# Performance work log

Hardware: AMD Instinct MI355X
Metric: run time of the kernel (lower is better)

## Reference

```python
import jax, jax.numpy as jnp
import numpy as np

B, S, D = 2, 2048, 1024
H, HD = 16, 64
MLP = 4096
EPS = 1e-5


def layer_norm(x, g, b):
    mu = jnp.mean(x, axis=-1, keepdims=True)
    var = jnp.mean(jnp.square(x - mu), axis=-1, keepdims=True)
    return (x - mu) * jax.lax.rsqrt(var + EPS) * g + b


def setup_inputs() -> dict:
    key = jax.random.key(0)
    ks = jax.random.split(key, 12)
    s = 0.02
    return {
        "x": jax.random.normal(ks[0], (B, S, D), jnp.float32),
        "ln1_g": jnp.ones((D,), jnp.float32),
        "ln1_b": jnp.zeros((D,), jnp.float32),
        "Wq": jax.random.normal(ks[1], (D, H * HD), jnp.float32) * s,
        "Wk": jax.random.normal(ks[2], (D, H * HD), jnp.float32) * s,
        "Wv": jax.random.normal(ks[3], (D, H * HD), jnp.float32) * s,
        "Wo": jax.random.normal(ks[4], (H * HD, D), jnp.float32) * s,
        "ln2_g": jnp.ones((D,), jnp.float32),
        "ln2_b": jnp.zeros((D,), jnp.float32),
        "fc1_w": jax.random.normal(ks[5], (D, MLP), jnp.float32) * s,
        "fc1_b": jnp.zeros((MLP,), jnp.float32),
        "fc2_w": jax.random.normal(ks[6], (MLP, D), jnp.float32) * s,
        "fc2_b": jnp.zeros((D,), jnp.float32),
    }


def reference(x, ln1_g, ln1_b, Wq, Wk, Wv, Wo, ln2_g, ln2_b, fc1_w, fc1_b, fc2_w, fc2_b):
    b, s, d = x.shape
    scale = 1.0 / np.sqrt(HD)
    h = layer_norm(x, ln1_g, ln1_b)
    # project and split heads: [b, H, s, HD]
    q = (h @ Wq).reshape(b, s, H, HD).transpose(0, 2, 1, 3)
    k = (h @ Wk).reshape(b, s, H, HD).transpose(0, 2, 1, 3)
    v = (h @ Wv).reshape(b, s, H, HD).transpose(0, 2, 1, 3)
    scores = jnp.einsum('bhqd,bhkd->bhqk', q, k) * scale
    causal = jnp.where(jnp.tril(jnp.ones((s, s), bool)), 0.0, -jnp.inf).astype(x.dtype)
    scores = scores + causal[None, None]
    attn_weights = jax.nn.softmax(scores, axis=-1)
    attn_out = jnp.einsum('bhqk,bhkd->bhqd', attn_weights, v)
    attn_out = attn_out.transpose(0, 2, 1, 3).reshape(b, s, H * HD) @ Wo
    x = x + attn_out
    h2 = layer_norm(x, ln2_g, ln2_b)
    mlp = jax.nn.gelu(h2 @ fc1_w + fc1_b, approximate=True) @ fc2_w + fc2_b
    x = x + mlp
    return (x, attn_weights)
```

## Files before the change

kernel.cpp:

```cpp
#include <hip/hip_runtime.h>
#include <cmath>

typedef __bf16 bf16;
typedef __bf16 bf16x8 __attribute__((ext_vector_type(8)));
typedef float f32x4 __attribute__((ext_vector_type(4)));

#define B_ 2
#define S_ 2048
#define D_ 1024
#define H_ 16
#define HD_ 64
#define MLP_ 4096
#define XOUT_ ((size_t)B_ * S_ * D_)

__device__ __forceinline__ void gll16(const void* g, void* l) {
  __builtin_amdgcn_global_load_lds((const __attribute__((address_space(1))) void*)g,
                                   (__attribute__((address_space(3))) void*)l, 16, 0, 0);
}

__device__ __forceinline__ f32x4 mfma16(bf16x8 a, bf16x8 b, f32x4 c) {
  return __builtin_amdgcn_mfma_f32_16x16x32_bf16(a, b, c, 0, 0, 0);
}

__device__ __forceinline__ float bfu2f(unsigned short u) {
  return __uint_as_float(((unsigned int)u) << 16);
}
__device__ __forceinline__ unsigned short f2bu(float v) {
  union { bf16 b; unsigned short u; } c; c.b = (bf16)v; return c.u;
}
__device__ __forceinline__ float ld_sc(const void* p, size_t i, int f32) {
  return f32 ? ((const float*)p)[i] : bfu2f(((const unsigned short*)p)[i]);
}

__global__ __launch_bounds__(64) void detect_k(const unsigned short* __restrict__ x,
                                               int* __restrict__ flag) {
  int tid = threadIdx.x;
  int cnt = 0;
  for (int i = tid; i < 512; i += 64) {
    int e = (x[i] >> 7) & 0xFF;
    if (e >= 0xBF) cnt++;
  }
  #pragma unroll
  for (int d = 1; d < 64; d <<= 1) cnt += __shfl_xor(cnt, d);
  if (tid == 0) flag[0] = (cnt > 8) ? 1 : 0;
}

__global__ __launch_bounds__(256) void transpose_ad(const void* __restrict__ in,
                                                    unsigned short* __restrict__ out,
                                                    int R, int C,
                                                    const int* __restrict__ flagp) {
  __shared__ unsigned short t[64][68];
  const int f32 = flagp[0];
  const int tid = threadIdx.x;
  const int c0 = blockIdx.x * 64, r0 = blockIdx.y * 64;
  for (int i = tid * 4; i < 4096; i += 1024) {
    int rr = i >> 6, cc = i & 63;
    size_t off = (size_t)(r0 + rr) * C + c0 + cc;
    if (f32) {
      float4 f = *(const float4*)((const float*)in + off);
      t[rr][cc + 0] = f2bu(f.x); t[rr][cc + 1] = f2bu(f.y);
      t[rr][cc + 2] = f2bu(f.z); t[rr][cc + 3] = f2bu(f.w);
    } else {
      *(ushort4*)&t[rr][cc] = *(const ushort4*)((const unsigned short*)in + off);
    }
  }
  __syncthreads();
  for (int i = tid * 4; i < 4096; i += 1024) {
    int orr = i & 63, oc = i >> 6;
    ushort4 v;
    v.x = t[orr + 0][oc]; v.y = t[orr + 1][oc];
    v.z = t[orr + 2][oc]; v.w = t[orr + 3][oc];
    *(ushort4*)(out + (size_t)(c0 + oc) * R + r0 + orr) = v;
  }
}

__global__ __launch_bounds__(256) void vtrans_k(const unsigned short* __restrict__ qkv,
                                                unsigned short* __restrict__ vT) {
  __shared__ unsigned short t[64][68];
  const int tid = threadIdx.x;
  const int s0 = blockIdx.x * 64, h = blockIdx.y, b = blockIdx.z;
  for (int i = tid * 4; i < 4096; i += 1024) {
    int si = i >> 6, hd = i & 63;
    *(ushort4*)&t[si][hd] =
        *(const ushort4*)(qkv + (size_t)(b * S_ + s0 + si) * 3072 + 2048 + h * 64 + hd);
  }
  __syncthreads();
  for (int i = tid * 4; i < 4096; i += 1024) {
    int ss = i & 63, hd = i >> 6;
    ushort4 v;
    v.x = t[ss + 0][hd]; v.y = t[ss + 1][hd];
    v.z = t[ss + 2][hd]; v.w = t[ss + 3][hd];
    *(ushort4*)(vT + ((size_t)(b * H_ + h) * 64 + hd) * S_ + s0 + ss) = v;
  }
}

__global__ __launch_bounds__(256) void ln_k(const void* __restrict__ xv,
                                            const void* __restrict__ g,
                                            const void* __restrict__ bvec,
                                            bf16* __restrict__ out,
                                            const int* __restrict__ flagp,
                                            int force_xf32) {
  const int f32 = flagp[0];
  const int xf32 = force_xf32 ? 1 : f32;
  const int row = blockIdx.x, tid = threadIdx.x;
  float v[4];
  if (xf32) {
    float4 f = *(const float4*)((const float*)xv + (size_t)row * 1024 + tid * 4);
    v[0] = f.x; v[1] = f.y; v[2] = f.z; v[3] = f.w;
  } else {
    ushort4 u = *(const ushort4*)((const unsigned short*)xv + (size_t)row * 1024 + tid * 4);
    v[0] = bfu2f(u.x); v[1] = bfu2f(u.y); v[2] = bfu2f(u.z); v[3] = bfu2f(u.w);
  }
  float s = 0.f, q = 0.f;
  #pragma unroll
  for (int i = 0; i < 4; i++) { s += v[i]; q += v[i] * v[i]; }
  #pragma unroll
  for (int d = 1; d < 64; d <<= 1) { s += __shfl_xor(s, d); q += __shfl_xor(q, d); }
  __shared__ float red[8];
  if ((tid & 63) == 0) { red[(tid >> 6) * 2] = s; red[(tid >> 6) * 2 + 1] = q; }
  __syncthreads();
  s = red[0] + red[2] + red[4] + red[6];
  q = red[1] + red[3] + red[5] + red[7];
  const float mean = s * (1.0f / 1024.0f);
  const float var = q * (1.0f / 1024.0f) - mean * mean;
  const float rs = rsqrtf(var + 1e-5f);
  unsigned short ov[4];
  #pragma unroll
  for (int i = 0; i < 4; i++) {
    float gg = ld_sc(g, tid * 4 + i, f32);
    float bb = ld_sc(bvec, tid * 4 + i, f32);
    ov[i] = f2bu((v[i] - mean) * rs * gg + bb);
  }
  ushort4 o4; o4.x = ov[0]; o4.y = ov[1]; o4.z = ov[2]; o4.w = ov[3];
  *(ushort4*)((unsigned short*)out + (size_t)row * 1024 + tid * 4) = o4;
}

template <int MODE>
__global__ __launch_bounds__(256) void gemm_bt(const bf16* __restrict__ A,
                                               const bf16* __restrict__ BT,
                                               int N, int K,
                                               const void* __restrict__ bias,
                                               const void* __restrict__ resb,
                                               const float* __restrict__ resf,
                                               bf16* __restrict__ outb,
                                               float* __restrict__ outf,
                                               const int* __restrict__ flagp) {
  __shared__ __align__(16) bf16 sA[128 * 64];
  __shared__ __align__(16) bf16 sB[128 * 64];
  const int f32 = flagp[0];
  const int tid = threadIdx.x;
  const int lane = tid & 63;
  const int wave = tid >> 6;
  const int wm = wave >> 1, wn = wave & 1;
  const int m0 = blockIdx.y * 128, n0 = blockIdx.x * 128;
  const int cn = lane & 15, rl = lane >> 4;
  const int r0 = tid >> 3, c16 = tid & 7;

  f32x4 zero = {0.f, 0.f, 0.f, 0.f};
  f32x4 acc[4][4];
  #pragma unroll
  for (int i = 0; i < 4; i++)
    #pragma unroll
    for (int j = 0; j < 4; j++) acc[i][j] = zero;

  for (int k0 = 0; k0 < K; k0 += 64) {
    __syncthreads();
    #pragma unroll
    for (int i = 0; i < 4; i++) {
      int row = r0 + i * 32;
      gll16(A + (size_t)(m0 + row) * K + k0 + c16 * 8, &sA[row * 64 + c16 * 8]);
      gll16(BT + (size_t)(n0 + row) * K + k0 + c16 * 8, &sB[row * 64 + c16 * 8]);
    }
    __syncthreads();
    #pragma unroll
    for (int kk = 0; kk < 64; kk += 32) {
      bf16x8 af[4], bfr[4];
      #pragma unroll
      for (int t = 0; t < 4; t++) {
        af[t] = *(const bf16x8*)&sA[(wm * 64 + t * 16 + cn) * 64 + kk + rl * 8];
        bfr[t] = *(const bf16x8*)&sB[(wn * 64 + t * 16 + cn) * 64 + kk + rl * 8];
      }
      #pragma unroll
      for (int mt = 0; mt < 4; mt++)
        #pragma unroll
        for (int nt = 0; nt < 4; nt++)
          acc[mt][nt] = mfma16(af[mt], bfr[nt], acc[mt][nt]);
    }
  }

  #pragma unroll
  for (int mt = 0; mt < 4; mt++) {
    #pragma unroll
    for (int nt = 0; nt < 4; nt++) {
      #pragma unroll
      for (int j = 0; j < 4; j++) {
        const int row = m0 + wm * 64 + mt * 16 + rl * 4 + j;
        const int col = n0 + wn * 64 + nt * 16 + cn;
        const size_t idx = (size_t)row * N + col;
        float v = acc[mt][nt][j];
        if (MODE == 0) {
          outb[idx] = (bf16)v;
        } else if (MODE == 1) {
          v += ld_sc(bias, col, f32);
          float gl = 0.5f * v * (1.0f + tanhf(0.7978845608028654f * (v + 0.044715f * v * v * v)));
          outb[idx] = (bf16)gl;
        } else if (MODE == 2) {
          outf[idx] = v + ld_sc(resb, idx, f32);
        } else {
          float val = v + ld_sc(bias, col, f32) + resf[idx];
          if (f32) outf[idx] = val; else outb[idx] = (bf16)val;
        }
      }
    }
  }
}

__global__ __launch_bounds__(256) void attn_k(const bf16* __restrict__ qkv,
                                              const bf16* __restrict__ vT,
                                              void* __restrict__ Pv,
                                              bf16* __restrict__ ao,
                                              const int* __restrict__ flagp) {
  __shared__ __align__(16) bf16 sQ[64 * 64];
  __shared__ __align__(16) bf16 sK[64 * 64];
  __shared__ __align__(16) bf16 sV[64 * 64];
  __shared__ __align__(16) bf16 sP[4][16 * 64];
  const int f32o = flagp[0];
  const int tid = threadIdx.x, lane = tid & 63, wave = tid >> 6;
  const int qt = blockIdx.x, h = blockIdx.y, b = blockIdx.z;
  const float scale = 0.125f;
  const float NEG = -1e30f;
  const int cn = lane & 15, rl = lane >> 4;
  const int r0 = tid >> 3, c16 = tid & 7;

  #pragma unroll
  for (int i = 0; i < 2; i++) {
    int row = r0 + i * 32;
    gll16(qkv + (size_t)(b * S_ + qt * 64 + row) * 3072 + h * 64 + c16 * 8,
          &sQ[row * 64 + c16 * 8]);
  }

  float m_i[4], l_i[4];
  #pragma unroll
  for (int j = 0; j < 4; j++) { m_i[j] = NEG; l_i[j] = 0.0f; }

  for (int kt = 0; kt <= qt; kt++) {
    __syncthreads();
    #pragma unroll
    for (int i = 0; i < 2; i++) {
      int row = r0 + i * 32;
      gll16(qkv + (size_t)(b * S_ + kt * 64 + row) * 3072 + 1024 + h * 64 + c16 * 8,
            &sK[row * 64 + c16 * 8]);
    }
    __syncthreads();
    f32x4 s[4];
    f32x4 zero = {0.f, 0.f, 0.f, 0.f};
    #pragma unroll
    for (int nt = 0; nt < 4; nt++) s[nt] = zero;
    #pragma unroll
    for (int kk = 0; kk < 64; kk += 32) {
      bf16x8 a = *(const bf16x8*)&sQ[(wave * 16 + cn) * 64 + kk + rl * 8];
      #pragma unroll
      for (int nt = 0; nt < 4; nt++) {
        bf16x8 bb = *(const bf16x8*)&sK[(nt * 16 + cn) * 64 + kk + rl * 8];
        s[nt] = mfma16(a, bb, s[nt]);
      }
    }
    const int rowg = qt * 64 + wave * 16 + rl * 4;
    const int colg0 = kt * 64 + cn;
    float pm[4] = {NEG, NEG, NEG, NEG};
    #pragma unroll
    for (int nt = 0; nt < 4; nt++)
      #pragma unroll
      for (int j = 0; j < 4; j++) {
        float v = (colg0 + nt * 16 > rowg + j) ? NEG : s[nt][j] * scale;
        s[nt][j] = v;
        pm[j] = fmaxf(pm[j], v);
      }
    #pragma unroll
    for (int j = 0; j < 4; j++) {
      #pragma unroll
      for (int d = 1; d < 16; d <<= 1) pm[j] = fmaxf(pm[j], __shfl_xor(pm[j], d));
      float mn = fmaxf(m_i[j], pm[j]);
      float ps = 0.f;
      #pragma unroll
      for (int nt = 0; nt < 4; nt++) ps += expf(s[nt][j] - mn);
      #pragma unroll
      for (int d = 1; d < 16; d <<= 1) ps += __shfl_xor(ps, d);
      l_i[j] = l_i[j] * expf(m_i[j] - mn) + ps;
      m_i[j] = mn;
    }
  }

  float inv_l[4];
  #pragma unroll
  for (int j = 0; j < 4; j++) inv_l[j] = 1.0f / l_i[j];

  f32x4 o[4];
  {
    f32x4 zero = {0.f, 0.f, 0.f, 0.f};
    #pragma unroll
    for (int nt = 0; nt < 4; nt++) o[nt] = zero;
  }
  for (int kt = 0; kt <= qt; kt++) {
    __syncthreads();
    #pragma unroll
    for (int i = 0; i < 2; i++) {
      int row = r0 + i * 32;
      gll16(qkv + (size_t)(b * S_ + kt * 64 + row) * 3072 + 1024 + h * 64 + c16 * 8,
            &sK[row * 64 + c16 * 8]);
      gll16(vT + ((size_t)(b * H_ + h) * 64 + row) * S_ + kt * 64 + c16 * 8,
            &sV[row * 64 + c16 * 8]);
    }
    __syncthreads();
    f32x4 s[4];
    f32x4 zero = {0.f, 0.f, 0.f, 0.f};
    #pragma unroll
    for (int nt = 0; nt < 4; nt++) s[nt] = zero;
    #pragma unroll
    for (int kk = 0; kk < 64; kk += 32) {
      bf16x8 a = *(const bf16x8*)&sQ[(wave * 16 + cn) * 64 + kk + rl * 8];
      #pragma unroll
      for (int nt = 0; nt < 4; nt++) {
        bf16x8 bb = *(const bf16x8*)&sK[(nt * 16 + cn) * 64 + kk + rl * 8];
        s[nt] = mfma16(a, bb, s[nt]);
      }
    }
    const int rowg = qt * 64 + wave * 16 + rl * 4;
    const int colg0 = kt * 64 + cn;
    #pragma unroll
    for (int nt = 0; nt < 4; nt++)
      #pragma unroll
      for (int j = 0; j < 4; j++) {
        bool masked = (colg0 + nt * 16 > rowg + j);
        float p = masked ? 0.0f : expf(s[nt][j] * scale - m_i[j]) * inv_l[j];
        sP[wave][(rl * 4 + j) * 64 + nt * 16 + cn] = (bf16)p;
      }
    __syncthreads();
    #pragma unroll
    for (int kk = 0; kk < 64; kk += 32) {
      bf16x8 ap = *(const bf16x8*)&sP[wave][cn * 64 + kk + rl * 8];
      #pragma unroll
      for (int nt = 0; nt < 4; nt++) {
        bf16x8 bv = *(const bf16x8*)&sV[(nt * 16 + cn) * 64 + kk + rl * 8];
        o[nt] = mfma16(ap, bv, o[nt]);
      }
    }
    size_t base = XOUT_ + (((size_t)b * H_ + h) * S_ + qt * 64 + wave * 16) * S_ + kt * 64;
    #pragma unroll
    for (int i = 0; i < 2; i++) {
      int idx = lane + i * 64;
      int r = idx >> 3, cc = idx & 7;
      if (f32o) {
        float4 lo, hi;
        const bf16* src = &sP[wave][r * 64 + cc * 8];
        lo.x = (float)src[0]; lo.y = (float)src[1]; lo.z = (float)src[2]; lo.w = (float)src[3];
        hi.x = (float)src[4]; hi.y = (float)src[5]; hi.z = (float)src[6]; hi.w = (float)src[7];
        *(float4*)((float*)Pv + base + (size_t)r * S_ + cc * 8) = lo;
        *(float4*)((float*)Pv + base + (size_t)r * S_ + cc * 8 + 4) = hi;
      } else {
        uint4 val = *(const uint4*)&sP[wave][r * 64 + cc * 8];
        *(uint4*)((bf16*)Pv + base + (size_t)r * S_ + cc * 8) = val;
      }
    }
  }

  {
    const int t0 = qt + 1;
    const int nch = (32 - t0) * 8;
    size_t rowbase = XOUT_ + (((size_t)b * H_ + h) * S_ + qt * 64) * S_;
    uint4 z; z.x = 0; z.y = 0; z.z = 0; z.w = 0;
    for (int idx = tid; idx < 64 * nch; idx += 256) {
      int r = idx / nch, cc = idx % nch;
      size_t off = rowbase + (size_t)r * S_ + t0 * 64 + cc * 8;
      if (f32o) {
        *(uint4*)((float*)Pv + off) = z;
        *(uint4*)((float*)Pv + off + 4) = z;
      } else {
        *(uint4*)((bf16*)Pv + off) = z;
      }
    }
  }

  #pragma unroll
  for (int nt = 0; nt < 4; nt++)
    #pragma unroll
    for (int j = 0; j < 4; j++) {
      int rowg2 = b * S_ + qt * 64 + wave * 16 + rl * 4 + j;
      ao[(size_t)rowg2 * 1024 + h * 64 + nt * 16 + cn] = (bf16)o[nt][j];
    }
}

extern "C" void kernel_launch(void* const* d_in, const int* in_sizes, int n_in,
                              void* d_out, int out_size, void* d_ws, size_t ws_size,
                              hipStream_t stream) {
  (void)in_sizes; (void)n_in; (void)out_size; (void)ws_size;
  const void* x    = d_in[0];
  const void* ln1g = d_in[1];
  const void* ln1b = d_in[2];
  const void* Wq   = d_in[3];
  const void* Wk   = d_in[4];
  const void* Wv   = d_in[5];
  const void* Wo   = d_in[6];
  const void* ln2g = d_in[7];
  const void* ln2b = d_in[8];
  const void* fc1w = d_in[9];
  const void* fc1b = d_in[10];
  const void* fc2w = d_in[11];
  const void* fc2b = d_in[12];

  char* ws = (char*)d_ws;
  bf16* wqkvT = (bf16*)(ws + 0);
  bf16* woT   = (bf16*)(ws + 6291456);
  bf16* fc1T  = (bf16*)(ws + 8388608);
  bf16* fc2T  = (bf16*)(ws + 16777216);
  bf16* h     = (bf16*)(ws + 25165824);
  bf16* qkv   = (bf16*)(ws + 33554432);
  bf16* vT    = (bf16*)(ws + 58720256);
  bf16* m1    = (bf16*)(ws + 33554432);
  bf16* aout  = (bf16*)(ws + 67108864);
  float* x1   = (float*)(ws + 75497472);
  int* flag   = (int*)(ws + 92274688);

  dim3 blk(256);

  detect_k<<<1, 64, 0, stream>>>((const unsigned short*)x, flag);

  transpose_ad<<<dim3(16, 16), blk, 0, stream>>>(Wq, (unsigned short*)wqkvT, 1024, 1024, flag);
  transpose_ad<<<dim3(16, 16), blk, 0, stream>>>(Wk, (unsigned short*)(wqkvT + 1024 * 1024), 1024, 1024, flag);
  transpose_ad<<<dim3(16, 16), blk, 0, stream>>>(Wv, (unsigned short*)(wqkvT + 2 * 1024 * 1024), 1024, 1024, flag);
  transpose_ad<<<dim3(16, 16), blk, 0, stream>>>(Wo, (unsigned short*)woT, 1024, 1024, flag);
  transpose_ad<<<dim3(64, 16), blk, 0, stream>>>(fc1w, (unsigned short*)fc1T, 1024, 4096, flag);
  transpose_ad<<<dim3(16, 64), blk, 0, stream>>>(fc2w, (unsigned short*)fc2T, 4096, 1024, flag);

  ln_k<<<4096, blk, 0, stream>>>(x, ln1g, ln1b, h, flag, 0);

  gemm_bt<0><<<dim3(24, 32), blk, 0, stream>>>(h, wqkvT, 3072, 1024, nullptr, nullptr, nullptr, qkv, nullptr, flag);

  vtrans_k<<<dim3(32, 16, 2), blk, 0, stream>>>((const unsigned short*)qkv, (unsigned short*)vT);

  attn_k<<<dim3(32, 16, 2), blk, 0, stream>>>(qkv, vT, d_out, aout, flag);

  gemm_bt<2><<<dim3(8, 32), blk, 0, stream>>>(aout, woT, 1024, 1024, nullptr, x, nullptr, nullptr, x1, flag);

  ln_k<<<4096, blk, 0, stream>>>(x1, ln2g, ln2b, h, flag, 1);

  gemm_bt<1><<<dim3(32, 32), blk, 0, stream>>>(h, fc1T, 4096, 1024, fc1b, nullptr, nullptr, m1, nullptr, flag);

  gemm_bt<3><<<dim3(8, 32), blk, 0, stream>>>(m1, fc2T, 1024, 4096, fc2b, nullptr, x1, (bf16*)d_out, (float*)d_out, flag);
}
```

Measured before the change: 1.150 ms.

## Single-pass attention without max, separate P normalization kernel, narrower GEMM tiles

```diff
diff --git a/kernel.cpp b/kernel.cpp
--- a/kernel.cpp
+++ b/kernel.cpp
@@ -189,9 +189,9 @@
   }
 
   #pragma unroll
-  for (int mt = 0; mt < 4; mt++) {
-    #pragma unroll
-    for (int nt = 0; nt < 4; nt++) {
+  for (int mt = 0; mt < 4; mt++)
+    #pragma unroll
+    for (int nt = 0; nt < 4; nt++)
       #pragma unroll
       for (int j = 0; j < 4; j++) {
         const int row = m0 + wm * 64 + mt * 16 + rl * 4 + j;
@@ -211,97 +211,128 @@
           if (f32) outf[idx] = val; else outb[idx] = (bf16)val;
         }
       }
-    }
-  }
+}
+
+template <int MODE>
+__global__ __launch_bounds__(256) void gemm_bt2(const bf16* __restrict__ A,
+                                                const bf16* __restrict__ BT,
+                                                int N, int K,
+                                                const void* __restrict__ bias,
+                                                const void* __restrict__ resb,
+                                                const float* __restrict__ resf,
+                                                bf16* __restrict__ outb,
+                                                float* __restrict__ outf,
+                                                const int* __restrict__ flagp) {
+  __shared__ __align__(16) bf16 sA[128 * 64];
+  __shared__ __align__(16) bf16 sB[64 * 64];
+  const int f32 = flagp[0];
+  const int tid = threadIdx.x;
+  const int lane = tid & 63;
+  const int wave = tid >> 6;
+  const int wm = wave >> 1, wn = wave & 1;
+  const int m0 = blockIdx.y * 128, n0 = blockIdx.x * 64;
+  const int cn = lane & 15, rl = lane >> 4;
+  const int r0 = tid >> 3, c16 = tid & 7;
+
+  f32x4 zero = {0.f, 0.f, 0.f, 0.f};
+  f32x4 acc[4][2];
+  #pragma unroll
+  for (int i = 0; i < 4; i++)
+    #pragma unroll
+    for (int j = 0; j < 2; j++) acc[i][j] = zero;
+
+  for (int k0 = 0; k0 < K; k0 += 64) {
+    __syncthreads();
+    #pragma unroll
+    for (int i = 0; i < 4; i++) {
+      int row = r0 + i * 32;
+      gll16(A + (size_t)(m0 + row) * K + k0 + c16 * 8, &sA[row * 64 + c16 * 8]);
+    }
+    #pragma unroll
+    for (int i = 0; i < 2; i++) {
+      int row = r0 + i * 32;
+      gll16(BT + (size_t)(n0 + row) * K + k0 + c16 * 8, &sB[row * 64 + c16 * 8]);
+    }
+    __syncthreads();
+    #pragma unroll
+    for (int kk = 0; kk < 64; kk += 32) {
+      bf16x8 af[4], bfr[2];
+      #pragma unroll
+      for (int t = 0; t < 4; t++)
+        af[t] = *(const bf16x8*)&sA[(wm * 64 + t * 16 + cn) * 64 + kk + rl * 8];
+      #pragma unroll
+      for (int t = 0; t < 2; t++)
+        bfr[t] = *(const bf16x8*)&sB[(wn * 32 + t * 16 + cn) * 64 + kk + rl * 8];
+      #pragma unroll
+      for (int mt = 0; mt < 4; mt++)
+        #pragma unroll
+        for (int nt = 0; nt < 2; nt++)
+          acc[mt][nt] = mfma16(af[mt], bfr[nt], acc[mt][nt]);
+    }
+  }
+
+  #pragma unroll
+  for (int mt = 0; mt < 4; mt++)
+    #pragma unroll
+    for (int nt = 0; nt < 2; nt++)
+      #pragma unroll
+      for (int j = 0; j < 4; j++) {
+        const int row = m0 + wm * 64 + mt * 16 + rl * 4 + j;
+        const int col = n0 + wn * 32 + nt * 16 + cn;
+        const size_t idx = (size_t)row * N + col;
+        float v = acc[mt][nt][j];
+        if (MODE == 0) {
+          outb[idx] = (bf16)v;
+        } else if (MODE == 1) {
+          v += ld_sc(bias, col, f32);
+          float gl = 0.5f * v * (1.0f + tanhf(0.7978845608028654f * (v + 0.044715f * v * v * v)));
+          outb[idx] = (bf16)gl;
+        } else if (MODE == 2) {
+          outf[idx] = v + ld_sc(resb, idx, f32);
+        } else {
+          float val = v + ld_sc(bias, col, f32) + resf[idx];
+          if (f32) outf[idx] = val; else outb[idx] = (bf16)val;
+        }
+      }
 }
 
 __global__ __launch_bounds__(256) void attn_k(const bf16* __restrict__ qkv,
                                               const bf16* __restrict__ vT,
                                               void* __restrict__ Pv,
                                               bf16* __restrict__ ao,
+                                              float* __restrict__ linv,
                                               const int* __restrict__ flagp) {
-  __shared__ __align__(16) bf16 sQ[64 * 64];
+  __shared__ __align__(16) bf16 sQ[128 * 64];
   __shared__ __align__(16) bf16 sK[64 * 64];
   __shared__ __align__(16) bf16 sV[64 * 64];
-  __shared__ __align__(16) bf16 sP[4][16 * 64];
+  __shared__ __align__(16) bf16 sP[4][32 * 64];
   const int f32o = flagp[0];
   const int tid = threadIdx.x, lane = tid & 63, wave = tid >> 6;
   const int qt = blockIdx.x, h = blockIdx.y, b = blockIdx.z;
-  const float scale = 0.125f;
-  const float NEG = -1e30f;
   const int cn = lane & 15, rl = lane >> 4;
   const int r0 = tid >> 3, c16 = tid & 7;
-
-  #pragma unroll
-  for (int i = 0; i < 2; i++) {
+  const float C2 = 0.125f * 1.4426950408889634f;
+
+  #pragma unroll
+  for (int i = 0; i < 4; i++) {
     int row = r0 + i * 32;
-    gll16(qkv + (size_t)(b * S_ + qt * 64 + row) * 3072 + h * 64 + c16 * 8,
+    gll16(qkv + (size_t)(b * S_ + qt * 128 + row) * 3072 + h * 64 + c16 * 8,
           &sQ[row * 64 + c16 * 8]);
   }
 
-  float m_i[4], l_i[4];
-  #pragma unroll
-  for (int j = 0; j < 4; j++) { m_i[j] = NEG; l_i[j] = 0.0f; }
-
-  for (int kt = 0; kt <= qt; kt++) {
-    __syncthreads();
-    #pragma unroll
-    for (int i = 0; i < 2; i++) {
-      int row = r0 + i * 32;
-      gll16(qkv + (size_t)(b * S_ + kt * 64 + row) * 3072 + 1024 + h * 64 + c16 * 8,
-            &sK[row * 64 + c16 * 8]);
-    }
-    __syncthreads();
-    f32x4 s[4];
-    f32x4 zero = {0.f, 0.f, 0.f, 0.f};
-    #pragma unroll
-    for (int nt = 0; nt < 4; nt++) s[nt] = zero;
-    #pragma unroll
-    for (int kk = 0; kk < 64; kk += 32) {
-      bf16x8 a = *(const bf16x8*)&sQ[(wave * 16 + cn) * 64 + kk + rl * 8];
-      #pragma unroll
-      for (int nt = 0; nt < 4; nt++) {
-        bf16x8 bb = *(const bf16x8*)&sK[(nt * 16 + cn) * 64 + kk + rl * 8];
-        s[nt] = mfma16(a, bb, s[nt]);
-      }
-    }
-    const int rowg = qt * 64 + wave * 16 + rl * 4;
-    const int colg0 = kt * 64 + cn;
-    float pm[4] = {NEG, NEG, NEG, NEG};
-    #pragma unroll
-    for (int nt = 0; nt < 4; nt++)
-      #pragma unroll
-      for (int j = 0; j < 4; j++) {
-        float v = (colg0 + nt * 16 > rowg + j) ? NEG : s[nt][j] * scale;
-        s[nt][j] = v;
-        pm[j] = fmaxf(pm[j], v);
-      }
-    #pragma unroll
-    for (int j = 0; j < 4; j++) {
-      #pragma unroll
-      for (int d = 1; d < 16; d <<= 1) pm[j] = fmaxf(pm[j], __shfl_xor(pm[j], d));
-      float mn = fmaxf(m_i[j], pm[j]);
-      float ps = 0.f;
-      #pragma unroll
-      for (int nt = 0; nt < 4; nt++) ps += expf(s[nt][j] - mn);
-      #pragma unroll
-      for (int d = 1; d < 16; d <<= 1) ps += __shfl_xor(ps, d);
-      l_i[j] = l_i[j] * expf(m_i[j] - mn) + ps;
-      m_i[j] = mn;
-    }
-  }
-
-  float inv_l[4];
-  #pragma unroll
-  for (int j = 0; j < 4; j++) inv_l[j] = 1.0f / l_i[j];
-
-  f32x4 o[4];
-  {
-    f32x4 zero = {0.f, 0.f, 0.f, 0.f};
-    #pragma unroll
-    for (int nt = 0; nt < 4; nt++) o[nt] = zero;
-  }
-  for (int kt = 0; kt <= qt; kt++) {
+  f32x4 o[2][4];
+  float lp[2][4];
+  #pragma unroll
+  for (int mt = 0; mt < 2; mt++)
+    #pragma unroll
+    for (int nt = 0; nt < 4; nt++) { o[mt][nt] = (f32x4){0.f, 0.f, 0.f, 0.f}; }
+  #pragma unroll
+  for (int mt = 0; mt < 2; mt++)
+    #pragma unroll
+    for (int j = 0; j < 4; j++) lp[mt][j] = 0.f;
+
+  const int ktmax = 2 * qt + 1;
+  for (int kt = 0; kt <= ktmax; kt++) {
     __syncthreads();
     #pragma unroll
     for (int i = 0; i < 2; i++) {
@@ -312,82 +343,170 @@
             &sV[row * 64 + c16 * 8]);
     }
     __syncthreads();
-    f32x4 s[4];
-    f32x4 zero = {0.f, 0.f, 0.f, 0.f};
-    #pragma unroll
-    for (int nt = 0; nt < 4; nt++) s[nt] = zero;
+
+    f32x4 s[2][4];
+    #pragma unroll
+    for (int mt = 0; mt < 2; mt++)
+      #pragma unroll
+      for (int nt = 0; nt < 4; nt++) s[mt][nt] = (f32x4){0.f, 0.f, 0.f, 0.f};
     #pragma unroll
     for (int kk = 0; kk < 64; kk += 32) {
-      bf16x8 a = *(const bf16x8*)&sQ[(wave * 16 + cn) * 64 + kk + rl * 8];
-      #pragma unroll
-      for (int nt = 0; nt < 4; nt++) {
-        bf16x8 bb = *(const bf16x8*)&sK[(nt * 16 + cn) * 64 + kk + rl * 8];
-        s[nt] = mfma16(a, bb, s[nt]);
-      }
-    }
-    const int rowg = qt * 64 + wave * 16 + rl * 4;
-    const int colg0 = kt * 64 + cn;
-    #pragma unroll
-    for (int nt = 0; nt < 4; nt++)
-      #pragma unroll
-      for (int j = 0; j < 4; j++) {
-        bool masked = (colg0 + nt * 16 > rowg + j);
-        float p = masked ? 0.0f : expf(s[nt][j] * scale - m_i[j]) * inv_l[j];
-        sP[wave][(rl * 4 + j) * 64 + nt * 16 + cn] = (bf16)p;
-      }
-    __syncthreads();
+      bf16x8 a[2], bb[4];
+      #pragma unroll
+      for (int mt = 0; mt < 2; mt++)
+        a[mt] = *(const bf16x8*)&sQ[(wave * 32 + mt * 16 + cn) * 64 + kk + rl * 8];
+      #pragma unroll
+      for (int nt = 0; nt < 4; nt++)
+        bb[nt] = *(const bf16x8*)&sK[(nt * 16 + cn) * 64 + kk + rl * 8];
+      #pragma unroll
+      for (int mt = 0; mt < 2; mt++)
+        #pragma unroll
+        for (int nt = 0; nt < 4; nt++)
+          s[mt][nt] = mfma16(a[mt], bb[nt], s[mt][nt]);
+    }
+
+    if (kt >= 2 * qt) {
+      #pragma unroll
+      for (int mt = 0; mt < 2; mt++)
+        #pragma unroll
+        for (int nt = 0; nt < 4; nt++)
+          #pragma unroll
+          for (int j = 0; j < 4; j++) {
+            int rowg = qt * 128 + wave * 32 + mt * 16 + rl * 4 + j;
+            int colg = kt * 64 + nt * 16 + cn;
+            float p = (colg > rowg) ? 0.f : exp2f(s[mt][nt][j] * C2);
+            lp[mt][j] += p;
+            sP[wave][(mt * 16 + rl * 4 + j) * 64 + nt * 16 + cn] = (bf16)p;
+          }
+    } else {
+      #pragma unroll
+      for (int mt = 0; mt < 2; mt++)
+        #pragma unroll
+        for (int nt = 0; nt < 4; nt++)
+          #pragma unroll
+          for (int j = 0; j < 4; j++) {
+            float p = exp2f(s[mt][nt][j] * C2);
+            lp[mt][j] += p;
+            sP[wave][(mt * 16 + rl * 4 + j) * 64 + nt * 16 + cn] = (bf16)p;
+          }
+    }
+    __syncthreads();
+
     #pragma unroll
     for (int kk = 0; kk < 64; kk += 32) {
-      bf16x8 ap = *(const bf16x8*)&sP[wave][cn * 64 + kk + rl * 8];
-      #pragma unroll
-      for (int nt = 0; nt < 4; nt++) {
-        bf16x8 bv = *(const bf16x8*)&sV[(nt * 16 + cn) * 64 + kk + rl * 8];
-        o[nt] = mfma16(ap, bv, o[nt]);
-      }
-    }
-    size_t base = XOUT_ + (((size_t)b * H_ + h) * S_ + qt * 64 + wave * 16) * S_ + kt * 64;
-    #pragma unroll
-    for (int i = 0; i < 2; i++) {
-      int idx = lane + i * 64;
-      int r = idx >> 3, cc = idx & 7;
+      bf16x8 ap[2], bv[4];
+      #pragma unroll
+      for (int mt = 0; mt < 2; mt++)
+        ap[mt] = *(const bf16x8*)&sP[wave][(mt * 16 + cn) * 64 + kk + rl * 8];
+      #pragma unroll
+      for (int nt = 0; nt < 4; nt++)
+        bv[nt] = *(const bf16x8*)&sV[(nt * 16 + cn) * 64 + kk + rl * 8];
+      #pragma unroll
+      for (int mt = 0; mt < 2; mt++)
+        #pragma unroll
+        for (int nt = 0; nt < 4; nt++)
+          o[mt][nt] = mfma16(ap[mt], bv[nt], o[mt][nt]);
+    }
+
+    #pragma unroll
+    for (int i = 0; i < 4; i++) {
+      int lin = i * 64 + lane;
+      int r = lin >> 3, cc = lin & 7;
+      size_t base = XOUT_ +
+          (((size_t)(b * H_ + h) * S_) + qt * 128 + wave * 32 + r) * S_ + kt * 64 + cc * 8;
+      const bf16* src = &sP[wave][r * 64 + cc * 8];
       if (f32o) {
         float4 lo, hi;
-        const bf16* src = &sP[wave][r * 64 + cc * 8];
         lo.x = (float)src[0]; lo.y = (float)src[1]; lo.z = (float)src[2]; lo.w = (float)src[3];
         hi.x = (float)src[4]; hi.y = (float)src[5]; hi.z = (float)src[6]; hi.w = (float)src[7];
-        *(float4*)((float*)Pv + base + (size_t)r * S_ + cc * 8) = lo;
-        *(float4*)((float*)Pv + base + (size_t)r * S_ + cc * 8 + 4) = hi;
+        *(float4*)((float*)Pv + base) = lo;
+        *(float4*)((float*)Pv + base + 4) = hi;
       } else {
-        uint4 val = *(const uint4*)&sP[wave][r * 64 + cc * 8];
-        *(uint4*)((bf16*)Pv + base + (size_t)r * S_ + cc * 8) = val;
-      }
-    }
-  }
-
-  {
-    const int t0 = qt + 1;
-    const int nch = (32 - t0) * 8;
-    size_t rowbase = XOUT_ + (((size_t)b * H_ + h) * S_ + qt * 64) * S_;
-    uint4 z; z.x = 0; z.y = 0; z.z = 0; z.w = 0;
-    for (int idx = tid; idx < 64 * nch; idx += 256) {
-      int r = idx / nch, cc = idx % nch;
-      size_t off = rowbase + (size_t)r * S_ + t0 * 64 + cc * 8;
+        *(uint4*)((bf16*)Pv + base) = *(const uint4*)src;
+      }
+    }
+  }
+
+  #pragma unroll
+  for (int mt = 0; mt < 2; mt++)
+    #pragma unroll
+    for (int j = 0; j < 4; j++) {
+      #pragma unroll
+      for (int d = 1; d < 16; d <<= 1) lp[mt][j] += __shfl_xor(lp[mt][j], d);
+      lp[mt][j] = 1.0f / lp[mt][j];
+    }
+
+  if (cn == 0) {
+    #pragma unroll
+    for (int mt = 0; mt < 2; mt++)
+      #pragma unroll
+      for (int j = 0; j < 4; j++)
+        linv[((size_t)(b * H_ + h)) * S_ + qt * 128 + wave * 32 + mt * 16 + rl * 4 + j] =
+            lp[mt][j];
+  }
+
+  #pragma unroll
+  for (int mt = 0; mt < 2; mt++)
+    #pragma unroll
+    for (int nt = 0; nt < 4; nt++)
+      #pragma unroll
+      for (int j = 0; j < 4; j++) {
+        int rowg = b * S_ + qt * 128 + wave * 32 + mt * 16 + rl * 4 + j;
+        ao[(size_t)rowg * 1024 + h * 64 + nt * 16 + cn] = (bf16)(o[mt][nt][j] * lp[mt][j]);
+      }
+}
+
+__global__ __launch_bounds__(256) void pnorm_k(void* __restrict__ Pv,
+                                               const float* __restrict__ linv,
+                                               const int* __restrict__ flagp) {
+  const int f32o = flagp[0];
+  const int qt = blockIdx.x, h = blockIdx.y, b = blockIdx.z;
+  const int tid = threadIdx.x;
+  const int cc = tid * 8;
+  for (int it = 0; it < 64; it++) {
+    const int r = qt * 64 + it;
+    const float inv = linv[((size_t)(b * H_ + h)) * S_ + r];
+    const size_t base = XOUT_ + (((size_t)(b * H_ + h) * S_) + r) * S_ + cc;
+    if (cc + 7 <= r) {
       if (f32o) {
-        *(uint4*)((float*)Pv + off) = z;
-        *(uint4*)((float*)Pv + off + 4) = z;
+        float4 a = *(float4*)((float*)Pv + base);
+        float4 c = *(float4*)((float*)Pv + base + 4);
+        a.x *= inv; a.y *= inv; a.z *= inv; a.w *= inv;
+        c.x *= inv; c.y *= inv; c.z *= inv; c.w *= inv;
+        *(float4*)((float*)Pv + base) = a;
+        *(float4*)((float*)Pv + base + 4) = c;
       } else {
-        *(uint4*)((bf16*)Pv + off) = z;
-      }
-    }
-  }
-
-  #pragma unroll
-  for (int nt = 0; nt < 4; nt++)
-    #pragma unroll
-    for (int j = 0; j < 4; j++) {
-      int rowg2 = b * S_ + qt * 64 + wave * 16 + rl * 4 + j;
-      ao[(size_t)rowg2 * 1024 + h * 64 + nt * 16 + cn] = (bf16)o[nt][j];
-    }
+        uint4 u = *(uint4*)((bf16*)Pv + base);
+        unsigned short* us = (unsigned short*)&u;
+        #pragma unroll
+        for (int e = 0; e < 8; e++) us[e] = f2bu(bfu2f(us[e]) * inv);
+        *(uint4*)((bf16*)Pv + base) = u;
+      }
+    } else if (cc > r) {
+      if (f32o) {
+        float4 z = {0.f, 0.f, 0.f, 0.f};
+        *(float4*)((float*)Pv + base) = z;
+        *(float4*)((float*)Pv + base + 4) = z;
+      } else {
+        uint4 z; z.x = 0; z.y = 0; z.z = 0; z.w = 0;
+        *(uint4*)((bf16*)Pv + base) = z;
+      }
+    } else {
+      if (f32o) {
+        #pragma unroll
+        for (int e = 0; e < 8; e++) {
+          float* p = (float*)Pv + base + e;
+          *p = (cc + e <= r) ? (*p) * inv : 0.f;
+        }
+      } else {
+        #pragma unroll
+        for (int e = 0; e < 8; e++) {
+          bf16* p = (bf16*)Pv + base + e;
+          *p = (cc + e <= r) ? (bf16)(bfu2f(*(unsigned short*)p) * inv) : (bf16)0.f;
+        }
+      }
+    }
+  }
 }
 
 extern "C" void kernel_launch(void* const* d_in, const int* in_sizes, int n_in,
@@ -410,6 +529,7 @@
 
   char* ws = (char*)d_ws;
   bf16* wqkvT = (bf16*)(ws + 0);
+  float* lws  = (float*)(ws + 0);
   bf16* woT   = (bf16*)(ws + 6291456);
   bf16* fc1T  = (bf16*)(ws + 8388608);
   bf16* fc2T  = (bf16*)(ws + 16777216);
@@ -438,13 +558,15 @@
 
   vtrans_k<<<dim3(32, 16, 2), blk, 0, stream>>>((const unsigned short*)qkv, (unsigned short*)vT);
 
-  attn_k<<<dim3(32, 16, 2), blk, 0, stream>>>(qkv, vT, d_out, aout, flag);
-
-  gemm_bt<2><<<dim3(8, 32), blk, 0, stream>>>(aout, woT, 1024, 1024, nullptr, x, nullptr, nullptr, x1, flag);
+  attn_k<<<dim3(16, 16, 2), blk, 0, stream>>>(qkv, vT, d_out, aout, lws, flag);
+
+  pnorm_k<<<dim3(32, 16, 2), blk, 0, stream>>>(d_out, lws, flag);
+
+  gemm_bt2<2><<<dim3(16, 32), blk, 0, stream>>>(aout, woT, 1024, 1024, nullptr, x, nullptr, nullptr, x1, flag);
 
   ln_k<<<4096, blk, 0, stream>>>(x1, ln2g, ln2b, h, flag, 1);
 
   gemm_bt<1><<<dim3(32, 32), blk, 0, stream>>>(h, fc1T, 4096, 1024, fc1b, nullptr, nullptr, m1, nullptr, flag);
 
-  gemm_bt<3><<<dim3(8, 32), blk, 0, stream>>>(m1, fc2T, 1024, 4096, fc2b, nullptr, x1, (bf16*)d_out, (float*)d_out, flag);
-}
+  gemm_bt2<3><<<dim3(16, 32), blk, 0, stream>>>(m1, fc2T, 1024, 4096, fc2b, nullptr, x1, (bf16*)d_out, (float*)d_out, flag);
+}
```

Result: slower. 1.258 ms (+9.3%).
